# Kernel optimization log

Hardware: AMD Instinct MI355X
Metric: run time of the kernel (lower is better)

The kernel has to match this reference:

```python
import jax, jax.numpy as jnp
import numpy as np

B = 65536
TEXT_DIM, USER_DIM, E, H, OUT_DIM = 768, 256, 128, 4, 256
LN_EPS = 1e-5


def _mha_seq1(q_in, kv_in, ipw, ipb, opw, opb):
    """nn.MultiheadAttention with query/key/value of seq_len=1 (batch_first).
    q_in, kv_in: [B, E]. ipw: [3E, E] packed q/k/v in_proj, opw: [E, E]."""
    wq, wk, wv = ipw[:E], ipw[E:2 * E], ipw[2 * E:]
    bq, bk, bv = ipb[:E], ipb[E:2 * E], ipb[2 * E:]
    q = q_in @ wq.T + bq                       # [B, E]
    k = kv_in @ wk.T + bk
    v = kv_in @ wv.T + bv
    hd = E // H
    qh = q.reshape(-1, H, hd)                  # [B, H, hd]
    kh = k.reshape(-1, H, hd)
    vh = v.reshape(-1, H, hd)
    # single key -> scores [B, H, 1]; softmax over the length-1 key axis == 1
    scores = jnp.sum(qh * kh, axis=-1, keepdims=True) / jnp.sqrt(jnp.float32(hd))
    w = jax.nn.softmax(scores, axis=-1)        # exactly ones
    attn = (w * vh).reshape(-1, E)             # [B, E]
    return attn @ opw.T + opb


def setup_inputs() -> dict:
    key = jax.random.key(0)
    ks = jax.random.split(key, 20)
    s = 0.02
    return {
        "text_features": jax.random.normal(ks[0], (B, TEXT_DIM), jnp.float32),
        "user_features": jax.random.normal(ks[1], (B, USER_DIM), jnp.float32),
        "tm_w": jax.random.normal(ks[2], (E, TEXT_DIM), jnp.float32) * s,
        "tm_b": jnp.zeros((E,), jnp.float32),
        "um_w": jax.random.normal(ks[3], (E, USER_DIM), jnp.float32) * s,
        "um_b": jnp.zeros((E,), jnp.float32),
        # stacked MHA params: 0=text_self, 1=user_self, 2=text_to_user, 3=user_to_text
        "ipw": jax.random.normal(ks[4], (4, 3 * E, E), jnp.float32) * s,
        "ipb": jnp.zeros((4, 3 * E), jnp.float32),
        "opw": jax.random.normal(ks[5], (4, E, E), jnp.float32) * s,
        "opb": jnp.zeros((4, E), jnp.float32),
        "tg_w": jax.random.normal(ks[6], (E, 2 * E), jnp.float32) * s,
        "tg_b": jnp.zeros((E,), jnp.float32),
        "ug_w": jax.random.normal(ks[7], (E, 2 * E), jnp.float32) * s,
        "ug_b": jnp.zeros((E,), jnp.float32),
        "ff_w": jax.random.normal(ks[8], (OUT_DIM, 2 * E), jnp.float32) * s,
        "ff_b": jnp.zeros((OUT_DIM,), jnp.float32),
        "ln_g": jnp.ones((OUT_DIM,), jnp.float32),
        "ln_b": jnp.zeros((OUT_DIM,), jnp.float32),
    }


def reference(text_features, user_features, tm_w, tm_b, um_w, um_b,
              ipw, ipb, opw, opb, tg_w, tg_b, ug_w, ug_b,
              ff_w, ff_b, ln_g, ln_b):
    text_m = text_features @ tm_w.T + tm_b     # [B, E]
    user_m = user_features @ um_w.T + um_b     # [B, E]

    text_self = _mha_seq1(text_m, text_m, ipw[0], ipb[0], opw[0], opb[0])
    user_self = _mha_seq1(user_m, user_m, ipw[1], ipb[1], opw[1], opb[1])
    text_cross = _mha_seq1(text_m, user_m, ipw[2], ipb[2], opw[2], opb[2])
    user_cross = _mha_seq1(user_m, text_m, ipw[3], ipb[3], opw[3], opb[3])

    tg = jax.nn.sigmoid(jnp.concatenate([text_self, text_cross], axis=1) @ tg_w.T + tg_b)
    ug = jax.nn.sigmoid(jnp.concatenate([user_self, user_cross], axis=1) @ ug_w.T + ug_b)

    text_final = text_self * (1 - tg) + text_cross * tg
    user_final = user_self * (1 - ug) + user_cross * ug

    fused = jnp.concatenate([text_final, user_final], axis=1)   # [B, 2E]
    h = fused @ ff_w.T + ff_b                                   # [B, OUT_DIM]
    mu = jnp.mean(h, axis=-1, keepdims=True)
    var = jnp.mean((h - mu) ** 2, axis=-1, keepdims=True)
    h = (h - mu) / jnp.sqrt(var + LN_EPS) * ln_g + ln_b
    return jax.nn.relu(h)  # Dropout(0.3) is identity in eval mode
```

## Files before the change

### kernel.cpp

```cpp
#include <hip/hip_runtime.h>
#include <hip/hip_bf16.h>


namespace {

typedef __attribute__((ext_vector_type(8))) short short8v;
typedef __attribute__((ext_vector_type(4))) float floatx4;

constexpr int OFF_CW  = 0;
constexpr int OFF_CB  = 262144;
constexpr int OFF_BT  = 264192;
constexpr int OFF_BU  = 265216;
constexpr int OFF_MTH = 266240;
constexpr int OFF_MTL = 659456;
constexpr int OFF_MUH = 1052672;
constexpr int OFF_MUL = 1183744;
constexpr int OFF_GW4 = 1314816;
constexpr int OFF_FW4 = 1576960;
constexpr int OFF_MT4 = 1839104;
constexpr int OFF_MU4 = 2625536;
constexpr int OFF_GTH = 2887680;
constexpr int OFF_GUH = 3280896;
constexpr int OFF_GB2 = 3411968;
constexpr long OFF_F  = 3412992;
constexpr long WS_NEED = OFF_F + 67108864L;

__device__ inline unsigned short f2b(float f) {
  __hip_bfloat16 h = __float2bfloat16(f);
  return __builtin_bit_cast(unsigned short, h);
}
__device__ inline float b2f(unsigned short u) {
  unsigned int v = ((unsigned int)u) << 16;
  return __builtin_bit_cast(float, v);
}
__device__ inline void split2(float v, unsigned short& h, unsigned short& l) {
  h = f2b(v);
  l = f2b(v - b2f(h));
}


__global__ void k_combine(const float* __restrict__ ipw, const float* __restrict__ opw,
                          char* __restrict__ wsb) {
  float* cw = (float*)(wsb + OFF_CW);
  int n = blockIdx.x * 256 + threadIdx.x;
  int i = n >> 14, o = (n >> 7) & 127, d = n & 127;
  const float* op = opw + i * 16384 + o * 128;
  const float* iv = ipw + i * 49152 + 256 * 128 + d;
  float s = 0.f;
#pragma unroll 4
  for (int m = 0; m < 128; ++m) s = fmaf(op[m], iv[m * 128], s);
  cw[i * 16384 + d * 128 + o] = s;
}

__global__ void k_combine_bias(const float* __restrict__ ipb, const float* __restrict__ opb,
                               const float* __restrict__ opw, char* __restrict__ wsb) {
  float* cb = (float*)(wsb + OFF_CB);
  int t = blockIdx.x * 256 + threadIdx.x;
  int i = t >> 7, o = t & 127;
  const float* op = opw + i * 16384 + o * 128;
  const float* ib = ipb + i * 384 + 256;
  float s = opb[i * 128 + o];
#pragma unroll 4
  for (int m = 0; m < 128; ++m) s = fmaf(op[m], ib[m], s);
  cb[t] = s;
}

__global__ void k_mt_hl(const float* __restrict__ tm_w, char* __restrict__ wsb) {
  const float* cw = (const float*)(wsb + OFF_CW);
  unsigned short* dh = (unsigned short*)(wsb + OFF_MTH);
  unsigned short* dl = (unsigned short*)(wsb + OFF_MTL);
  int n = blockIdx.x * 256 + threadIdx.x;
  int k = n >> 8, c = n & 255;
  const float* p = cw + ((c >> 7) ? 3 : 0) * 16384 + (c & 127);
  float s = 0.f;
#pragma unroll 4
  for (int d = 0; d < 128; ++d) s = fmaf(p[d * 128], tm_w[d * 768 + k], s);
  unsigned short h, l;
  split2(s, h, l);
  int ofs = (((k >> 3) * 256 + c) << 3) + (k & 7);
  dh[ofs] = h;
  dl[ofs] = l;
}

__global__ void k_mu_hl(const float* __restrict__ um_w, char* __restrict__ wsb) {
  const float* cw = (const float*)(wsb + OFF_CW);
  unsigned short* dh = (unsigned short*)(wsb + OFF_MUH);
  unsigned short* dl = (unsigned short*)(wsb + OFF_MUL);
  int n = blockIdx.x * 256 + threadIdx.x;
  int k = n >> 8, c = n & 255;
  const float* p = cw + ((c >> 7) ? 1 : 2) * 16384 + (c & 127);
  float s = 0.f;
#pragma unroll 4
  for (int d = 0; d < 128; ++d) s = fmaf(p[d * 128], um_w[d * 256 + k], s);
  unsigned short h, l;
  split2(s, h, l);
  int ofs = (((k >> 3) * 256 + c) << 3) + (k & 7);
  dh[ofs] = h;
  dl[ofs] = l;
}

__global__ void k_mt4(const float* __restrict__ tm_w, char* __restrict__ wsb) {
  const float* cw = (const float*)(wsb + OFF_CW);
  float* dst = (float*)(wsb + OFF_MT4);
  int n = blockIdx.x * 256 + threadIdx.x;
  int k = n >> 8, c = n & 255;
  const float* p = cw + ((c >> 7) ? 3 : 0) * 16384 + (c & 127);
  float s = 0.f;
#pragma unroll 4
  for (int d = 0; d < 128; ++d) s = fmaf(p[d * 128], tm_w[d * 768 + k], s);
  dst[(((k >> 2) * 256 + c) << 2) + (k & 3)] = s;
}

__global__ void k_mu4(const float* __restrict__ um_w, char* __restrict__ wsb) {
  const float* cw = (const float*)(wsb + OFF_CW);
  float* dst = (float*)(wsb + OFF_MU4);
  int n = blockIdx.x * 256 + threadIdx.x;
  int k = n >> 8, c = n & 255;
  const float* p = cw + ((c >> 7) ? 1 : 2) * 16384 + (c & 127);
  float s = 0.f;
#pragma unroll 4
  for (int d = 0; d < 128; ++d) s = fmaf(p[d * 128], um_w[d * 256 + k], s);
  dst[(((k >> 2) * 256 + c) << 2) + (k & 3)] = s;
}

__global__ void k_bias_tu(const float* __restrict__ tm_b, const float* __restrict__ um_b,
                          char* __restrict__ wsb) {
  const float* cw = (const float*)(wsb + OFF_CW);
  const float* cb = (const float*)(wsb + OFF_CB);
  float* bT = (float*)(wsb + OFF_BT);
  float* bU = (float*)(wsb + OFF_BU);
  int t = blockIdx.x * 256 + threadIdx.x;
  if (t < 256) {
    int sel = (t >> 7) ? 3 : 0;
    const float* p = cw + sel * 16384 + (t & 127);
    float s = cb[sel * 128 + (t & 127)];
#pragma unroll 4
    for (int d = 0; d < 128; ++d) s = fmaf(p[d * 128], tm_b[d], s);
    bT[t] = s;
  } else {
    int c = t - 256;
    int sel = (c >> 7) ? 1 : 2;
    const float* p = cw + sel * 16384 + (c & 127);
    float s = cb[sel * 128 + (c & 127)];
#pragma unroll 4
    for (int d = 0; d < 128; ++d) s = fmaf(p[d * 128], um_b[d], s);
    bU[c] = s;
  }
}

__global__ void k_gt(const float* __restrict__ tg_w, const float* __restrict__ ug_w,
                     char* __restrict__ wsb) {
  const float* mt = (const float*)(wsb + OFF_MT4);
  unsigned short* dst = (unsigned short*)(wsb + OFF_GTH);
  int idx = blockIdx.x * 256 + threadIdx.x;
  int k = idx >> 8, n = idx & 255;
  const float* mb = mt + (((k >> 2) * 256) << 2) + (k & 3);
  float s = 0.f;
  if (n < 128) {
    const float* w = tg_w + n * 256;
#pragma unroll 4
    for (int m = 0; m < 128; ++m) s = fmaf(w[m], mb[m * 4], s);
  } else {
    const float* w = ug_w + (n - 128) * 256 + 128;
#pragma unroll 4
    for (int m = 0; m < 128; ++m) s = fmaf(w[m], mb[(128 + m) * 4], s);
  }
  dst[(((k >> 3) * 256 + n) << 3) + (k & 7)] = f2b(s);
}

__global__ void k_gu(const float* __restrict__ tg_w, const float* __restrict__ ug_w,
                     char* __restrict__ wsb) {
  const float* mu = (const float*)(wsb + OFF_MU4);
  unsigned short* dst = (unsigned short*)(wsb + OFF_GUH);
  int idx = blockIdx.x * 256 + threadIdx.x;
  int k = idx >> 8, n = idx & 255;
  const float* mb = mu + (((k >> 2) * 256) << 2) + (k & 3);
  float s = 0.f;
  if (n < 128) {
    const float* w = tg_w + n * 256 + 128;
#pragma unroll 4
    for (int m = 0; m < 128; ++m) s = fmaf(w[m], mb[m * 4], s);
  } else {
    const float* w = ug_w + (n - 128) * 256;
#pragma unroll 4
    for (int m = 0; m < 128; ++m) s = fmaf(w[m], mb[(128 + m) * 4], s);
  }
  dst[(((k >> 3) * 256 + n) << 3) + (k & 7)] = f2b(s);
}

__global__ void k_gbias(const float* __restrict__ tg_w, const float* __restrict__ tg_b,
                        const float* __restrict__ ug_w, const float* __restrict__ ug_b,
                        char* __restrict__ wsb) {
  const float* bT = (const float*)(wsb + OFF_BT);
  const float* bU = (const float*)(wsb + OFF_BU);
  float* gb2 = (float*)(wsb + OFF_GB2);
  int n = threadIdx.x;
  float s;
  if (n < 128) {
    s = tg_b[n];
    const float* w = tg_w + n * 256;
#pragma unroll 4
    for (int m = 0; m < 128; ++m) s = fmaf(w[m], bT[m], s);
#pragma unroll 4
    for (int m = 0; m < 128; ++m) s = fmaf(w[128 + m], bU[m], s);
  } else {
    int np = n - 128;
    s = ug_b[np];
    const float* w = ug_w + np * 256;
#pragma unroll 4
    for (int m = 0; m < 128; ++m) s = fmaf(w[m], bU[128 + m], s);
#pragma unroll 4
    for (int m = 0; m < 128; ++m) s = fmaf(w[128 + m], bT[128 + m], s);
  }
  gb2[n] = s;
}

__global__ void k_pack_gw4(const float* __restrict__ tg_w, const float* __restrict__ ug_w,
                           char* __restrict__ wsb) {
  float* dst = (float*)(wsb + OFF_GW4);
  int idx = blockIdx.x * 256 + threadIdx.x;
  int j = idx >> 8, n = idx & 255;
  float v = (n < 128) ? tg_w[n * 256 + j] : ug_w[(n - 128) * 256 + j];
  dst[(((j >> 2) * 256 + n) << 2) + (j & 3)] = v;
}

__global__ void k_transpose4(const float* __restrict__ src, float* __restrict__ dst,
                             int R, int C) {
  int n = blockIdx.x * 256 + threadIdx.x;
  if (n >= R * C) return;
  int o = n / C, k = n % C;
  dst[(((k >> 2) * R + o) << 2) + (k & 3)] = src[n];
}


#define SWZ(byte, row) ((byte) ^ (((row) & 7) << 4))

__launch_bounds__(512)
__global__ void k_s12g(const float* __restrict__ xt_g, const float* __restrict__ xu_g,
                       const char* __restrict__ wsb, float* __restrict__ Fg) {
  __shared__ __align__(16) char sm[65536];
  constexpr int XTL = 24576;
  constexpr int XUH = 49152;
  constexpr int XUL = 57344;

  const int t = threadIdx.x;
  const int wave = t >> 6, lane = t & 63;
  const int lrow = lane & 15;
  const int lk8 = lane >> 4;
  const int n0w = wave * 32;
  const long row0 = (long)blockIdx.x * 32;

  const float* bT = (const float*)(wsb + OFF_BT);
  const float* bU = (const float*)(wsb + OFF_BU);
  const float* gb2 = (const float*)(wsb + OFF_GB2);

  floatx4 zero = {0.f, 0.f, 0.f, 0.f};
  floatx4 acc1[2][2] = {{zero, zero}, {zero, zero}};
  floatx4 acc2[2][2] = {{zero, zero}, {zero, zero}};
  floatx4 accG1[2][2] = {{zero, zero}, {zero, zero}};
  floatx4 accG2[2][2] = {{zero, zero}, {zero, zero}};

  for (int p = 0; p < 2; ++p) {
    if (p) __syncthreads();

#pragma unroll
    for (int it = 0; it < 6; ++it) {
      int idx = it * 512 + t;
      int row = idx / 96, rem = idx - row * 96;
      float4 v = *(const float4*)(xt_g + (row0 + row) * 768 + p * 384 + rem * 4);
      int b0 = row * 768 + rem * 8;
      ushort4 hh, ll;
      split2(v.x, hh.x, ll.x); split2(v.y, hh.y, ll.y);
      split2(v.z, hh.z, ll.z); split2(v.w, hh.w, ll.w);
      *(ushort4*)(sm + SWZ(b0, row)) = hh;
      *(ushort4*)(sm + XTL + SWZ(b0, row)) = ll;
    }
#pragma unroll
    for (int it = 0; it < 2; ++it) {
      int idx = it * 512 + t;
      int row = idx >> 5, rem = idx & 31;
      float4 v = *(const float4*)(xu_g + (row0 + row) * 256 + p * 128 + rem * 4);
      int b0 = row * 256 + rem * 8;
      ushort4 hh, ll;
      split2(v.x, hh.x, ll.x); split2(v.y, hh.y, ll.y);
      split2(v.z, hh.z, ll.z); split2(v.w, hh.w, ll.w);
      *(ushort4*)(sm + XUH + SWZ(b0, row)) = hh;
      *(ushort4*)(sm + XUL + SWZ(b0, row)) = ll;
    }
    __syncthreads();

    {
      const char* wh = wsb + OFF_MTH;
      const char* wl = wsb + OFF_MTL;
      const char* gt = wsb + OFF_GTH;
#pragma unroll 4
      for (int kk = 0; kk < 384; kk += 32) {
        int kb = (kk + lk8 * 8) * 2;
        int k8 = ((p * 384 + kk) >> 3) + lk8;
        int o0 = (k8 * 256 + n0w + lrow) << 4;
        int o1 = (k8 * 256 + n0w + 16 + lrow) << 4;
        short8v bh0 = *(const short8v*)(wh + o0);
        short8v bh1 = *(const short8v*)(wh + o1);
        short8v bl0 = *(const short8v*)(wl + o0);
        short8v bl1 = *(const short8v*)(wl + o1);
        short8v g0 = *(const short8v*)(gt + o0);
        short8v g1 = *(const short8v*)(gt + o1);
#pragma unroll
        for (int rg = 0; rg < 2; ++rg) {
          int ar = rg * 16 + lrow;
          short8v ah = *(const short8v*)(sm + SWZ(ar * 768 + kb, ar));
          short8v al = *(const short8v*)(sm + XTL + SWZ(ar * 768 + kb, ar));
          acc1[rg][0] = __builtin_amdgcn_mfma_f32_16x16x32_bf16(ah, bh0, acc1[rg][0], 0, 0, 0);
          acc1[rg][0] = __builtin_amdgcn_mfma_f32_16x16x32_bf16(ah, bl0, acc1[rg][0], 0, 0, 0);
          acc1[rg][0] = __builtin_amdgcn_mfma_f32_16x16x32_bf16(al, bh0, acc1[rg][0], 0, 0, 0);
          acc1[rg][1] = __builtin_amdgcn_mfma_f32_16x16x32_bf16(ah, bh1, acc1[rg][1], 0, 0, 0);
          acc1[rg][1] = __builtin_amdgcn_mfma_f32_16x16x32_bf16(ah, bl1, acc1[rg][1], 0, 0, 0);
          acc1[rg][1] = __builtin_amdgcn_mfma_f32_16x16x32_bf16(al, bh1, acc1[rg][1], 0, 0, 0);
          accG1[rg][0] = __builtin_amdgcn_mfma_f32_16x16x32_bf16(ah, g0, accG1[rg][0], 0, 0, 0);
          accG1[rg][1] = __builtin_amdgcn_mfma_f32_16x16x32_bf16(ah, g1, accG1[rg][1], 0, 0, 0);
        }
      }
    }
    {
      const char* wh = wsb + OFF_MUH;
      const char* wl = wsb + OFF_MUL;
      const char* gu = wsb + OFF_GUH;
#pragma unroll
      for (int kk = 0; kk < 128; kk += 32) {
        int kb = (kk + lk8 * 8) * 2;
        int k8 = ((p * 128 + kk) >> 3) + lk8;
        int o0 = (k8 * 256 + n0w + lrow) << 4;
        int o1 = (k8 * 256 + n0w + 16 + lrow) << 4;
        short8v bh0 = *(const short8v*)(wh + o0);
        short8v bh1 = *(const short8v*)(wh + o1);
        short8v bl0 = *(const short8v*)(wl + o0);
        short8v bl1 = *(const short8v*)(wl + o1);
        short8v g0 = *(const short8v*)(gu + o0);
        short8v g1 = *(const short8v*)(gu + o1);
#pragma unroll
        for (int rg = 0; rg < 2; ++rg) {
          int ar = rg * 16 + lrow;
          short8v ah = *(const short8v*)(sm + XUH + SWZ(ar * 256 + kb, ar));
          short8v al = *(const short8v*)(sm + XUL + SWZ(ar * 256 + kb, ar));
          acc2[rg][0] = __builtin_amdgcn_mfma_f32_16x16x32_bf16(ah, bh0, acc2[rg][0], 0, 0, 0);
          acc2[rg][0] = __builtin_amdgcn_mfma_f32_16x16x32_bf16(ah, bl0, acc2[rg][0], 0, 0, 0);
          acc2[rg][0] = __builtin_amdgcn_mfma_f32_16x16x32_bf16(al, bh0, acc2[rg][0], 0, 0, 0);
          acc2[rg][1] = __builtin_amdgcn_mfma_f32_16x16x32_bf16(ah, bh1, acc2[rg][1], 0, 0, 0);
          acc2[rg][1] = __builtin_amdgcn_mfma_f32_16x16x32_bf16(ah, bl1, acc2[rg][1], 0, 0, 0);
          acc2[rg][1] = __builtin_amdgcn_mfma_f32_16x16x32_bf16(al, bh1, acc2[rg][1], 0, 0, 0);
          accG2[rg][0] = __builtin_amdgcn_mfma_f32_16x16x32_bf16(ah, g0, accG2[rg][0], 0, 0, 0);
          accG2[rg][1] = __builtin_amdgcn_mfma_f32_16x16x32_bf16(ah, g1, accG2[rg][1], 0, 0, 0);
        }
      }
    }
  }

#pragma unroll
  for (int rg = 0; rg < 2; ++rg)
#pragma unroll
    for (int nt = 0; nt < 2; ++nt) {
      int n = n0w + nt * 16 + lrow;
      float bvT = bT[n], bvU = bU[n], gbn = gb2[n];
#pragma unroll
      for (int reg = 0; reg < 4; ++reg) {
        long row = row0 + rg * 16 + lk8 * 4 + reg;
        float a1 = acc1[rg][nt][reg] + bvT;
        float a2 = acc2[rg][nt][reg] + bvU;
        float logit = accG1[rg][nt][reg] + accG2[rg][nt][reg] + gbn;
        float g = 1.f / (1.f + __expf(-logit));
        float f = (n < 128) ? fmaf(g, a2 - a1, a1)
                            : fmaf(g, a1 - a2, a2);
        Fg[row * 256 + n] = f;
      }
    }
}


__launch_bounds__(256)
__global__ void k_ffln(const float* __restrict__ Fg, const char* __restrict__ wsb,
                       const float* __restrict__ ff_b, const float* __restrict__ ln_g,
                       const float* __restrict__ ln_b, float* __restrict__ out) {
  __shared__ float lds[16 * 256 + 16 * 256];
  float* F = lds;
  float* H = lds + 4096;

  const int t = threadIdx.x;
  const long row0 = (long)blockIdx.x * 16;

  {
    const float4* g = (const float4*)(Fg + row0 * 256);
    float4* l = (float4*)F;
#pragma unroll
    for (int it = 0; it < 4; ++it) l[it * 256 + t] = g[it * 256 + t];
  }
  __syncthreads();

  const int rh = t >> 7, c0 = (t & 127) * 2;
  const int r0 = rh * 8;

  {
    const float4* FW = (const float4*)(wsb + OFF_FW4);
    float acc[8][2] = {};
    for (int j = 0; j < 256; j += 4) {
      float4 w0 = FW[(j >> 2) * 256 + c0];
      float4 w1 = FW[(j >> 2) * 256 + c0 + 1];
#pragma unroll
      for (int r = 0; r < 8; ++r) {
        float4 fv = *(const float4*)&F[(r0 + r) * 256 + j];
        acc[r][0] = fmaf(fv.x, w0.x, fmaf(fv.y, w0.y, fmaf(fv.z, w0.z, fmaf(fv.w, w0.w, acc[r][0]))));
        acc[r][1] = fmaf(fv.x, w1.x, fmaf(fv.y, w1.y, fmaf(fv.z, w1.z, fmaf(fv.w, w1.w, acc[r][1]))));
      }
    }
    float fb0 = ff_b[c0], fb1 = ff_b[c0 + 1];
#pragma unroll
    for (int r = 0; r < 8; ++r) {
      int row = r0 + r;
      H[row * 256 + c0]     = acc[r][0] + fb0;
      H[row * 256 + c0 + 1] = acc[r][1] + fb1;
    }
  }
  __syncthreads();

  {
    int r = t >> 4, q = t & 15;
    const float* Hr = H + r * 256 + q * 16;
    float4 hv[4];
    float s1 = 0.f, s2 = 0.f;
#pragma unroll
    for (int j = 0; j < 4; ++j) {
      hv[j] = *(const float4*)(Hr + j * 4);
      s1 += hv[j].x + hv[j].y + hv[j].z + hv[j].w;
      s2 += hv[j].x * hv[j].x + hv[j].y * hv[j].y + hv[j].z * hv[j].z + hv[j].w * hv[j].w;
    }
#pragma unroll
    for (int off = 1; off < 16; off <<= 1) {
      s1 += __shfl_xor(s1, off);
      s2 += __shfl_xor(s2, off);
    }
    float mu = s1 * (1.f / 256.f);
    float var = s2 * (1.f / 256.f) - mu * mu;
    float rstd = rsqrtf(var + 1e-5f);
    float* op = out + (row0 + r) * 256 + q * 16;
#pragma unroll
    for (int j = 0; j < 4; ++j) {
      const float* gp = ln_g + q * 16 + j * 4;
      const float* bp = ln_b + q * 16 + j * 4;
      float4 o;
      o.x = fmaf((hv[j].x - mu) * rstd, gp[0], bp[0]);
      o.y = fmaf((hv[j].y - mu) * rstd, gp[1], bp[1]);
      o.z = fmaf((hv[j].z - mu) * rstd, gp[2], bp[2]);
      o.w = fmaf((hv[j].w - mu) * rstd, gp[3], bp[3]);
      o.x = o.x > 0.f ? o.x : 0.f;
      o.y = o.y > 0.f ? o.y : 0.f;
      o.z = o.z > 0.f ? o.z : 0.f;
      o.w = o.w > 0.f ? o.w : 0.f;
      *(float4*)(op + j * 4) = o;
    }
  }
}


__launch_bounds__(256)
__global__ void k_main5(const float* __restrict__ xt_g, const float* __restrict__ xu_g,
                        const char* __restrict__ wsb,
                        const float* __restrict__ tg_b, const float* __restrict__ ug_b,
                        const float* __restrict__ ff_b, const float* __restrict__ ln_g,
                        const float* __restrict__ ln_b, float* __restrict__ out) {
  __shared__ float lds[8 * 768 + 8 * 512 + 8 * 256];
  float* xt = lds;
  float* S = lds + 8 * 768;
  float* xu = lds + 8 * 768 + 8 * 512;

  const int t = threadIdx.x;
  const long row0 = (long)blockIdx.x * 8;

  {
    const float4* g = (const float4*)(xt_g + row0 * 768);
    float4* l = (float4*)xt;
#pragma unroll
    for (int it = 0; it < 6; ++it) l[it * 256 + t] = g[it * 256 + t];
    const float4* gu = (const float4*)(xu_g + row0 * 256);
    float4* lu = (float4*)xu;
#pragma unroll
    for (int it = 0; it < 2; ++it) lu[it * 256 + t] = gu[it * 256 + t];
  }
  __syncthreads();

  {
    const float4* W4 = (const float4*)(wsb + OFF_MT4);
    float acc[8];
#pragma unroll
    for (int r = 0; r < 8; ++r) acc[r] = 0.f;
    for (int k = 0; k < 768; k += 4) {
      float4 w = W4[(k >> 2) * 256 + t];
#pragma unroll
      for (int r = 0; r < 8; ++r) {
        float4 xv = *(const float4*)&xt[r * 768 + k];
        acc[r] = fmaf(w.x, xv.x, acc[r]);
        acc[r] = fmaf(w.y, xv.y, acc[r]);
        acc[r] = fmaf(w.z, xv.z, acc[r]);
        acc[r] = fmaf(w.w, xv.w, acc[r]);
      }
    }
    float bias = ((const float*)(wsb + OFF_BT))[t];
    int d = (t < 128) ? t : (256 + t);
#pragma unroll
    for (int r = 0; r < 8; ++r) S[r * 512 + d] = acc[r] + bias;
  }

  {
    const float4* W4 = (const float4*)(wsb + OFF_MU4);
    float acc[8];
#pragma unroll
    for (int r = 0; r < 8; ++r) acc[r] = 0.f;
    for (int k = 0; k < 256; k += 4) {
      float4 w = W4[(k >> 2) * 256 + t];
#pragma unroll
      for (int r = 0; r < 8; ++r) {
        float4 xv = *(const float4*)&xu[r * 256 + k];
        acc[r] = fmaf(w.x, xv.x, acc[r]);
        acc[r] = fmaf(w.y, xv.y, acc[r]);
        acc[r] = fmaf(w.z, xv.z, acc[r]);
        acc[r] = fmaf(w.w, xv.w, acc[r]);
      }
    }
    float bias = ((const float*)(wsb + OFF_BU))[t];
#pragma unroll
    for (int r = 0; r < 8; ++r) S[r * 512 + 128 + t] = acc[r] + bias;
  }
  __syncthreads();

  {
    int c = t & 127, half = t >> 7;
    const float4* W4 = (const float4*)(wsb + OFF_GW4);
    const int wcol = half * 128 + c;
    const int so = half * 256;
    float acc[8];
#pragma unroll
    for (int r = 0; r < 8; ++r) acc[r] = 0.f;
    for (int j = 0; j < 256; j += 4) {
      float4 w = W4[(j >> 2) * 256 + wcol];
#pragma unroll
      for (int r = 0; r < 8; ++r) {
        float4 sv = *(const float4*)&S[r * 512 + so + j];
        acc[r] = fmaf(w.x, sv.x, acc[r]);
        acc[r] = fmaf(w.y, sv.y, acc[r]);
        acc[r] = fmaf(w.z, sv.z, acc[r]);
        acc[r] = fmaf(w.w, sv.w, acc[r]);
      }
    }
    float gb = half ? ug_b[c] : tg_b[c];
    float* F = xu;
#pragma unroll
    for (int r = 0; r < 8; ++r) {
      float g = 1.f / (1.f + __expf(-(acc[r] + gb)));
      float a = S[r * 512 + so + c];
      float b = S[r * 512 + so + 128 + c];
      F[r * 256 + half * 128 + c] = fmaf(g, b - a, a);
    }
  }
  __syncthreads();

  {
    const float4* W4 = (const float4*)(wsb + OFF_FW4);
    const float* F = xu;
    float acc[8];
#pragma unroll
    for (int r = 0; r < 8; ++r) acc[r] = 0.f;
    for (int j = 0; j < 256; j += 4) {
      float4 w = W4[(j >> 2) * 256 + t];
#pragma unroll
      for (int r = 0; r < 8; ++r) {
        float4 fv = *(const float4*)&F[r * 256 + j];
        acc[r] = fmaf(w.x, fv.x, acc[r]);
        acc[r] = fmaf(w.y, fv.y, acc[r]);
        acc[r] = fmaf(w.z, fv.z, acc[r]);
        acc[r] = fmaf(w.w, fv.w, acc[r]);
      }
    }
    float* H = xt;
    float bias = ff_b[t];
#pragma unroll
    for (int r = 0; r < 8; ++r) H[r * 256 + t] = acc[r] + bias;
  }
  __syncthreads();

  {
    const float* H = xt;
    int r = t >> 5, q = t & 31;
    const float* Hr = H + r * 256 + q * 8;
    float s1 = 0.f, s2 = 0.f;
#pragma unroll
    for (int i = 0; i < 8; ++i) {
      float v = Hr[i];
      s1 += v;
      s2 += v * v;
    }
#pragma unroll
    for (int off = 1; off < 32; off <<= 1) {
      s1 += __shfl_xor(s1, off);
      s2 += __shfl_xor(s2, off);
    }
    float mu = s1 * (1.f / 256.f);
    float var = s2 * (1.f / 256.f) - mu * mu;
    float rstd = rsqrtf(var + 1e-5f);
    float* op = out + (row0 + r) * 256 + q * 8;
#pragma unroll
    for (int i = 0; i < 8; ++i) {
      float v = (Hr[i] - mu) * rstd * ln_g[q * 8 + i] + ln_b[q * 8 + i];
      op[i] = v > 0.f ? v : 0.f;
    }
  }
}

}

extern "C" void kernel_launch(void* const* d_in, const int* in_sizes, int n_in,
                              void* d_out, int out_size, void* d_ws, size_t ws_size,
                              hipStream_t stream) {
  const float* text = (const float*)d_in[0];
  const float* user = (const float*)d_in[1];
  const float* tm_w = (const float*)d_in[2];
  const float* tm_b = (const float*)d_in[3];
  const float* um_w = (const float*)d_in[4];
  const float* um_b = (const float*)d_in[5];
  const float* ipw = (const float*)d_in[6];
  const float* ipb = (const float*)d_in[7];
  const float* opw = (const float*)d_in[8];
  const float* opb = (const float*)d_in[9];
  const float* tg_w = (const float*)d_in[10];
  const float* tg_b = (const float*)d_in[11];
  const float* ug_w = (const float*)d_in[12];
  const float* ug_b = (const float*)d_in[13];
  const float* ff_w = (const float*)d_in[14];
  const float* ff_b = (const float*)d_in[15];
  const float* ln_g = (const float*)d_in[16];
  const float* ln_b = (const float*)d_in[17];
  char* wsb = (char*)d_ws;
  float* out = (float*)d_out;

  k_combine<<<256, 256, 0, stream>>>(ipw, opw, wsb);
  k_combine_bias<<<2, 256, 0, stream>>>(ipb, opb, opw, wsb);
  k_bias_tu<<<2, 256, 0, stream>>>(tm_b, um_b, wsb);
  k_mt4<<<768, 256, 0, stream>>>(tm_w, wsb);
  k_mu4<<<256, 256, 0, stream>>>(um_w, wsb);
  k_transpose4<<<256, 256, 0, stream>>>(ff_w, (float*)(wsb + OFF_FW4), 256, 256);

  if ((long)ws_size >= WS_NEED) {
    float* Fg = (float*)(wsb + OFF_F);
    k_mt_hl<<<768, 256, 0, stream>>>(tm_w, wsb);
    k_mu_hl<<<256, 256, 0, stream>>>(um_w, wsb);
    k_gt<<<768, 256, 0, stream>>>(tg_w, ug_w, wsb);
    k_gu<<<256, 256, 0, stream>>>(tg_w, ug_w, wsb);
    k_gbias<<<1, 256, 0, stream>>>(tg_w, tg_b, ug_w, ug_b, wsb);
    k_s12g<<<2048, 512, 0, stream>>>(text, user, wsb, Fg);
    k_ffln<<<4096, 256, 0, stream>>>(Fg, wsb, ff_b, ln_g, ln_b, out);
  } else {
    k_pack_gw4<<<256, 256, 0, stream>>>(tg_w, ug_w, wsb);
    k_main5<<<8192, 256, 0, stream>>>(text, user, wsb, tg_b, ug_b, ff_b, ln_g, ln_b, out);
  }
}
```

Before: 500.1 us.

## Move final FF GEMM to split-bf16 MFMA kernel with separate LayerNorm pass

Replaces the scalar-FMA FF+LayerNorm kernel with two kernels. The first runs the 256x256 FF GEMM on MFMA using a three-product hi/lo bf16 split, which keeps near-fp32 accuracy, and writes the result back in place into the intermediate buffer. The second kernel does the LayerNorm and ReLU. The goal is to take the FP32 FMA-bound GEMM off the vector ALUs. The cost is an extra full read and write of the 64MB intermediate between the two kernels.

Result: faster. 420.3 us, median of 2 (-16.0%).

```diff
diff --git a/kernel.cpp b/kernel.cpp
--- a/kernel.cpp
+++ b/kernel.cpp
@@ -22,7 +22,9 @@
 constexpr int OFF_GTH = 2887680;
 constexpr int OFF_GUH = 3280896;
 constexpr int OFF_GB2 = 3411968;
-constexpr long OFF_F  = 3412992;
+constexpr int OFF_FFH = 3412992;
+constexpr int OFF_FFL = 3544064;
+constexpr long OFF_F  = 3675136;
 constexpr long WS_NEED = OFF_F + 67108864L;
 
 __device__ inline unsigned short f2b(float f) {
@@ -95,6 +97,18 @@
   unsigned short h, l;
   split2(s, h, l);
   int ofs = (((k >> 3) * 256 + c) << 3) + (k & 7);
+  dh[ofs] = h;
+  dl[ofs] = l;
+}
+
+__global__ void k_ff_hl(const float* __restrict__ ff_w, char* __restrict__ wsb) {
+  unsigned short* dh = (unsigned short*)(wsb + OFF_FFH);
+  unsigned short* dl = (unsigned short*)(wsb + OFF_FFL);
+  int idx = blockIdx.x * 256 + threadIdx.x;
+  int k = idx >> 8, n = idx & 255;
+  unsigned short h, l;
+  split2(ff_w[n * 256 + k], h, l);
+  int ofs = (((k >> 3) * 256 + n) << 3) + (k & 7);
   dh[ofs] = h;
   dl[ofs] = l;
 }
@@ -376,86 +390,117 @@
 }
 
 
+__launch_bounds__(512)
+__global__ void k_ff32(float* FHg, const char* __restrict__ wsb,
+                       const float* __restrict__ ff_b) {
+  __shared__ __align__(16) char sm[32768];
+  constexpr int FLO = 16384;
+
+  const int t = threadIdx.x;
+  const int wave = t >> 6, lane = t & 63;
+  const int lrow = lane & 15;
+  const int lk8 = lane >> 4;
+  const int n0w = wave * 32;
+  const long row0 = (long)blockIdx.x * 32;
+
+#pragma unroll
+  for (int it = 0; it < 4; ++it) {
+    int idx = it * 512 + t;
+    int row = idx >> 6, rem = idx & 63;
+    float4 v = *(const float4*)(FHg + (row0 + row) * 256 + rem * 4);
+    int b0 = row * 512 + rem * 8;
+    ushort4 hh, ll;
+    split2(v.x, hh.x, ll.x); split2(v.y, hh.y, ll.y);
+    split2(v.z, hh.z, ll.z); split2(v.w, hh.w, ll.w);
+    *(ushort4*)(sm + SWZ(b0, row)) = hh;
+    *(ushort4*)(sm + FLO + SWZ(b0, row)) = ll;
+  }
+  __syncthreads();
+
+  floatx4 zero = {0.f, 0.f, 0.f, 0.f};
+  floatx4 acc[2][2] = {{zero, zero}, {zero, zero}};
+
+  {
+    const char* wh = wsb + OFF_FFH;
+    const char* wl = wsb + OFF_FFL;
+#pragma unroll
+    for (int kk = 0; kk < 256; kk += 32) {
+      int kb = (kk + lk8 * 8) * 2;
+      int k8 = (kk >> 3) + lk8;
+      int o0 = (k8 * 256 + n0w + lrow) << 4;
+      int o1 = (k8 * 256 + n0w + 16 + lrow) << 4;
+      short8v bh0 = *(const short8v*)(wh + o0);
+      short8v bh1 = *(const short8v*)(wh + o1);
+      short8v bl0 = *(const short8v*)(wl + o0);
+      short8v bl1 = *(const short8v*)(wl + o1);
+#pragma unroll
+      for (int rg = 0; rg < 2; ++rg) {
+        int ar = rg * 16 + lrow;
+        short8v ah = *(const short8v*)(sm + SWZ(ar * 512 + kb, ar));
+        short8v al = *(const short8v*)(sm + FLO + SWZ(ar * 512 + kb, ar));
+        acc[rg][0] = __builtin_amdgcn_mfma_f32_16x16x32_bf16(ah, bh0, acc[rg][0], 0, 0, 0);
+        acc[rg][0] = __builtin_amdgcn_mfma_f32_16x16x32_bf16(ah, bl0, acc[rg][0], 0, 0, 0);
+        acc[rg][0] = __builtin_amdgcn_mfma_f32_16x16x32_bf16(al, bh0, acc[rg][0], 0, 0, 0);
+        acc[rg][1] = __builtin_amdgcn_mfma_f32_16x16x32_bf16(ah, bh1, acc[rg][1], 0, 0, 0);
+        acc[rg][1] = __builtin_amdgcn_mfma_f32_16x16x32_bf16(ah, bl1, acc[rg][1], 0, 0, 0);
+        acc[rg][1] = __builtin_amdgcn_mfma_f32_16x16x32_bf16(al, bh1, acc[rg][1], 0, 0, 0);
+      }
+    }
+  }
+
+#pragma unroll
+  for (int rg = 0; rg < 2; ++rg)
+#pragma unroll
+    for (int nt = 0; nt < 2; ++nt) {
+      int n = n0w + nt * 16 + lrow;
+      float fb = ff_b[n];
+#pragma unroll
+      for (int reg = 0; reg < 4; ++reg) {
+        long row = row0 + rg * 16 + lk8 * 4 + reg;
+        FHg[row * 256 + n] = acc[rg][nt][reg] + fb;
+      }
+    }
+}
+
+
 __launch_bounds__(256)
-__global__ void k_ffln(const float* __restrict__ Fg, const char* __restrict__ wsb,
-                       const float* __restrict__ ff_b, const float* __restrict__ ln_g,
-                       const float* __restrict__ ln_b, float* __restrict__ out) {
-  __shared__ float lds[16 * 256 + 16 * 256];
-  float* F = lds;
-  float* H = lds + 4096;
-
+__global__ void k_ln(const float* __restrict__ Hg, const float* __restrict__ ln_g,
+                     const float* __restrict__ ln_b, float* __restrict__ out) {
   const int t = threadIdx.x;
   const long row0 = (long)blockIdx.x * 16;
-
-  {
-    const float4* g = (const float4*)(Fg + row0 * 256);
-    float4* l = (float4*)F;
-#pragma unroll
-    for (int it = 0; it < 4; ++it) l[it * 256 + t] = g[it * 256 + t];
-  }
-  __syncthreads();
-
-  const int rh = t >> 7, c0 = (t & 127) * 2;
-  const int r0 = rh * 8;
-
-  {
-    const float4* FW = (const float4*)(wsb + OFF_FW4);
-    float acc[8][2] = {};
-    for (int j = 0; j < 256; j += 4) {
-      float4 w0 = FW[(j >> 2) * 256 + c0];
-      float4 w1 = FW[(j >> 2) * 256 + c0 + 1];
-#pragma unroll
-      for (int r = 0; r < 8; ++r) {
-        float4 fv = *(const float4*)&F[(r0 + r) * 256 + j];
-        acc[r][0] = fmaf(fv.x, w0.x, fmaf(fv.y, w0.y, fmaf(fv.z, w0.z, fmaf(fv.w, w0.w, acc[r][0]))));
-        acc[r][1] = fmaf(fv.x, w1.x, fmaf(fv.y, w1.y, fmaf(fv.z, w1.z, fmaf(fv.w, w1.w, acc[r][1]))));
-      }
-    }
-    float fb0 = ff_b[c0], fb1 = ff_b[c0 + 1];
-#pragma unroll
-    for (int r = 0; r < 8; ++r) {
-      int row = r0 + r;
-      H[row * 256 + c0]     = acc[r][0] + fb0;
-      H[row * 256 + c0 + 1] = acc[r][1] + fb1;
-    }
-  }
-  __syncthreads();
-
-  {
-    int r = t >> 4, q = t & 15;
-    const float* Hr = H + r * 256 + q * 16;
-    float4 hv[4];
-    float s1 = 0.f, s2 = 0.f;
-#pragma unroll
-    for (int j = 0; j < 4; ++j) {
-      hv[j] = *(const float4*)(Hr + j * 4);
-      s1 += hv[j].x + hv[j].y + hv[j].z + hv[j].w;
-      s2 += hv[j].x * hv[j].x + hv[j].y * hv[j].y + hv[j].z * hv[j].z + hv[j].w * hv[j].w;
-    }
-#pragma unroll
-    for (int off = 1; off < 16; off <<= 1) {
-      s1 += __shfl_xor(s1, off);
-      s2 += __shfl_xor(s2, off);
-    }
-    float mu = s1 * (1.f / 256.f);
-    float var = s2 * (1.f / 256.f) - mu * mu;
-    float rstd = rsqrtf(var + 1e-5f);
-    float* op = out + (row0 + r) * 256 + q * 16;
-#pragma unroll
-    for (int j = 0; j < 4; ++j) {
-      const float* gp = ln_g + q * 16 + j * 4;
-      const float* bp = ln_b + q * 16 + j * 4;
-      float4 o;
-      o.x = fmaf((hv[j].x - mu) * rstd, gp[0], bp[0]);
-      o.y = fmaf((hv[j].y - mu) * rstd, gp[1], bp[1]);
-      o.z = fmaf((hv[j].z - mu) * rstd, gp[2], bp[2]);
-      o.w = fmaf((hv[j].w - mu) * rstd, gp[3], bp[3]);
-      o.x = o.x > 0.f ? o.x : 0.f;
-      o.y = o.y > 0.f ? o.y : 0.f;
-      o.z = o.z > 0.f ? o.z : 0.f;
-      o.w = o.w > 0.f ? o.w : 0.f;
-      *(float4*)(op + j * 4) = o;
-    }
+  int r = t >> 4, q = t & 15;
+  const float* Hr = Hg + (row0 + r) * 256 + q * 16;
+  float4 hv[4];
+  float s1 = 0.f, s2 = 0.f;
+#pragma unroll
+  for (int j = 0; j < 4; ++j) {
+    hv[j] = *(const float4*)(Hr + j * 4);
+    s1 += hv[j].x + hv[j].y + hv[j].z + hv[j].w;
+    s2 += hv[j].x * hv[j].x + hv[j].y * hv[j].y + hv[j].z * hv[j].z + hv[j].w * hv[j].w;
+  }
+#pragma unroll
+  for (int off = 1; off < 16; off <<= 1) {
+    s1 += __shfl_xor(s1, off);
+    s2 += __shfl_xor(s2, off);
+  }
+  float mu = s1 * (1.f / 256.f);
+  float var = s2 * (1.f / 256.f) - mu * mu;
+  float rstd = rsqrtf(var + 1e-5f);
+  float* op = out + (row0 + r) * 256 + q * 16;
+#pragma unroll
+  for (int j = 0; j < 4; ++j) {
+    const float* gp = ln_g + q * 16 + j * 4;
+    const float* bp = ln_b + q * 16 + j * 4;
+    float4 o;
+    o.x = fmaf((hv[j].x - mu) * rstd, gp[0], bp[0]);
+    o.y = fmaf((hv[j].y - mu) * rstd, gp[1], bp[1]);
+    o.z = fmaf((hv[j].z - mu) * rstd, gp[2], bp[2]);
+    o.w = fmaf((hv[j].w - mu) * rstd, gp[3], bp[3]);
+    o.x = o.x > 0.f ? o.x : 0.f;
+    o.y = o.y > 0.f ? o.y : 0.f;
+    o.z = o.z > 0.f ? o.z : 0.f;
+    o.w = o.w > 0.f ? o.w : 0.f;
+    *(float4*)(op + j * 4) = o;
   }
 }
 
@@ -644,7 +689,6 @@
   k_bias_tu<<<2, 256, 0, stream>>>(tm_b, um_b, wsb);
   k_mt4<<<768, 256, 0, stream>>>(tm_w, wsb);
   k_mu4<<<256, 256, 0, stream>>>(um_w, wsb);
-  k_transpose4<<<256, 256, 0, stream>>>(ff_w, (float*)(wsb + OFF_FW4), 256, 256);
 
   if ((long)ws_size >= WS_NEED) {
     float* Fg = (float*)(wsb + OFF_F);
@@ -653,10 +697,13 @@
     k_gt<<<768, 256, 0, stream>>>(tg_w, ug_w, wsb);
     k_gu<<<256, 256, 0, stream>>>(tg_w, ug_w, wsb);
     k_gbias<<<1, 256, 0, stream>>>(tg_w, tg_b, ug_w, ug_b, wsb);
+    k_ff_hl<<<256, 256, 0, stream>>>(ff_w, wsb);
     k_s12g<<<2048, 512, 0, stream>>>(text, user, wsb, Fg);
-    k_ffln<<<4096, 256, 0, stream>>>(Fg, wsb, ff_b, ln_g, ln_b, out);
+    k_ff32<<<2048, 512, 0, stream>>>(Fg, wsb, ff_b);
+    k_ln<<<4096, 256, 0, stream>>>(Fg, ln_g, ln_b, out);
   } else {
     k_pack_gw4<<<256, 256, 0, stream>>>(tg_w, ug_w, wsb);
+    k_transpose4<<<256, 256, 0, stream>>>(ff_w, (float*)(wsb + OFF_FW4), 256, 256);
     k_main5<<<8192, 256, 0, stream>>>(text, user, wsb, tg_b, ug_b, ff_b, ln_g, ln_b, out);
   }
 }
```
